# Optimization experiments

Measured on AMD Instinct MI355X. Metric: run time of the kernel, lower is better.

Reference implementation:

```python
import jax, jax.numpy as jnp
import numpy as np

B, L, D_MODEL = 8, 1024, 512
D_STATE, D_CONV, EXPAND = 16, 4, 2
D_INNER = EXPAND * D_MODEL          # 1024
DT_RANK = (D_MODEL + 15) // 16      # 32
D_FF = 4 * D_MODEL                  # 2048
EPS = 1e-12


def setup_inputs() -> dict:
    key = jax.random.key(0)
    ks = jax.random.split(key, 16)
    s = 0.02
    n = lambda k, shp: jax.random.normal(k, shp, dtype=jnp.float32) * s
    A = jnp.tile(jnp.arange(1, D_STATE + 1, dtype=jnp.float32)[None, :], (D_INNER, 1))
    return {
        "x": jax.random.normal(ks[0], (B, L, D_MODEL), dtype=jnp.float32),
        "in_proj_w": n(ks[1], (2 * D_INNER, D_MODEL)),
        "conv_w": n(ks[2], (D_INNER, 1, D_CONV)),
        "conv_b": jnp.zeros((D_INNER,), jnp.float32),
        "x_proj_w": n(ks[3], (DT_RANK + 2 * D_STATE, D_INNER)),
        "dt_proj_w": n(ks[4], (D_INNER, DT_RANK)),
        "dt_proj_b": jnp.full((D_INNER,), -4.0, jnp.float32),  # softplus(~-4) -> small dt
        "A_log": jnp.log(A),
        "D": jnp.ones((D_INNER,), jnp.float32),
        "out_proj_w": n(ks[5], (D_MODEL, D_INNER)),
        "ln1_g": jnp.ones((D_MODEL,), jnp.float32),
        "ln1_b": jnp.zeros((D_MODEL,), jnp.float32),
        "fc1_w": n(ks[6], (D_FF, D_MODEL)),
        "fc1_b": jnp.zeros((D_FF,), jnp.float32),
        "fc2_w": n(ks[7], (D_MODEL, D_FF)),
        "fc2_b": jnp.zeros((D_MODEL,), jnp.float32),
        "ln2_g": jnp.ones((D_MODEL,), jnp.float32),
        "ln2_b": jnp.zeros((D_MODEL,), jnp.float32),
    }


def _layernorm(x, g, b):
    m = jnp.mean(x, axis=-1, keepdims=True)
    v = jnp.var(x, axis=-1, keepdims=True)
    return (x - m) * jax.lax.rsqrt(v + EPS) * g + b


def _mamba(x, in_proj_w, conv_w, conv_b, x_proj_w, dt_proj_w, dt_proj_b, A_log, D, out_proj_w):
    # in_proj: [B,L,d_model] -> [B,L,2*d_inner]
    xz = jnp.einsum("bld,ed->ble", x, in_proj_w)
    u, z = jnp.split(xz, 2, axis=-1)                      # each [B,L,d_inner]
    # depthwise causal conv over time
    uc = jax.lax.conv_general_dilated(
        jnp.transpose(u, (0, 2, 1)), conv_w,
        window_strides=(1,), padding=[(D_CONV - 1, 0)],
        feature_group_count=D_INNER,
        dimension_numbers=("NCH", "OIH", "NCH"))
    u = jnp.transpose(uc, (0, 2, 1)) + conv_b             # [B,L,d_inner]
    u = jax.nn.silu(u)
    # x_proj -> dt, B, C
    x_dbl = jnp.einsum("bld,ed->ble", u, x_proj_w)
    dt, Bm, Cm = jnp.split(x_dbl, [DT_RANK, DT_RANK + D_STATE], axis=-1)
    dt = jax.nn.softplus(jnp.einsum("blr,dr->bld", dt, dt_proj_w) + dt_proj_b)  # [B,L,d_inner]
    A = -jnp.exp(A_log)                                   # [d_inner, d_state]
    deltaA = jnp.exp(dt[..., None] * A)                   # [B,L,d_inner,d_state]
    deltaBu = dt[..., None] * Bm[:, :, None, :] * u[..., None]

    def step(h, inp):
        dA_t, dBu_t, C_t = inp                            # [B,di,ds],[B,di,ds],[B,ds]
        h = h * dA_t + dBu_t
        y = jnp.einsum("bds,bs->bd", h, C_t)
        return h, y

    h0 = jnp.zeros((x.shape[0], D_INNER, D_STATE), x.dtype)
    _, ys = jax.lax.scan(step, h0, (jnp.transpose(deltaA, (1, 0, 2, 3)),
                                    jnp.transpose(deltaBu, (1, 0, 2, 3)),
                                    jnp.transpose(Cm, (1, 0, 2))))
    y = jnp.transpose(ys, (1, 0, 2)) + u * D              # [B,L,d_inner]
    y = y * jax.nn.silu(z)
    return jnp.einsum("ble,de->bld", y, out_proj_w)


def reference(x, in_proj_w, conv_w, conv_b, x_proj_w, dt_proj_w, dt_proj_b, A_log, D,
              out_proj_w, ln1_g, ln1_b, fc1_w, fc1_b, fc2_w, fc2_b, ln2_g, ln2_b):
    h = _mamba(x, in_proj_w, conv_w, conv_b, x_proj_w, dt_proj_w, dt_proj_b,
               A_log, D, out_proj_w)
    h = _layernorm(h + x, ln1_g, ln1_b)                   # dropout = identity (eval)
    # FeedForward with residual + LayerNorm
    f = jax.nn.gelu(jnp.einsum("bld,fd->blf", h, fc1_w) + fc1_b, approximate=False)
    f = jnp.einsum("blf,df->bld", f, fc2_w) + fc2_b
    return _layernorm(f + h, ln2_g, ln2_b)
```

## Files before the change

kernel.cpp:

```cpp
#include <hip/hip_runtime.h>
#include <hip/hip_bf16.h>
#include <math.h>

typedef __hip_bfloat16 bf16;
typedef unsigned short u16;
typedef unsigned int u32;
typedef __attribute__((ext_vector_type(8))) short short8;
typedef __attribute__((ext_vector_type(4))) float f32x4;
typedef __attribute__((ext_vector_type(4))) u32 u32x4;

#define B_  8
#define L_  1024
#define DM  512
#define DI  1024
#define DS  16
#define DR  32
#define DF  2048
#define M_  (B_ * L_)

__device__ __forceinline__ float b2f(bf16 x) { return __bfloat162float(x); }
__device__ __forceinline__ bf16  f2b(float x) { return __float2bfloat16(x); }
__device__ __forceinline__ u16   bu(bf16 x)  { return __builtin_bit_cast(u16, x); }
__device__ __forceinline__ float s2f(short x) { return b2f(__builtin_bit_cast(bf16, (u16)x)); }
__device__ __forceinline__ float uphi(u32 w) { return __builtin_bit_cast(float, w & 0xffff0000u); }
__device__ __forceinline__ float uplo(u32 w) { return __builtin_bit_cast(float, w << 16); }

__device__ __forceinline__ bool is_b16(const void* flag) {
    return ((const u16*)flag)[0] == 0x3F80;
}
__device__ __forceinline__ float ldr(const void* p, size_t i, bool b16) {
    return b16 ? b2f(((const bf16*)p)[i]) : ((const float*)p)[i];
}

__device__ __forceinline__ float fexp2(float x) {
#if __has_builtin(__builtin_amdgcn_exp2f)
    return __builtin_amdgcn_exp2f(x);
#else
    return __expf(x * 0.6931471805599453f);
#endif
}

__device__ __forceinline__ float fsoftplus(float v) {
    return (v > 20.f) ? v : __logf(1.f + __expf(v));
}

__device__ __forceinline__ float fgelu(float v) {
    const float x = v * 0.7071067811865475f;
    const float ax = fabsf(x);
    const float t = __builtin_amdgcn_rcpf(fmaf(0.3275911f, ax, 1.f));
    float p = fmaf(1.061405429f, t, -1.453152027f);
    p = fmaf(p, t, 1.421413741f);
    p = fmaf(p, t, -0.284496736f);
    p = fmaf(p, t, 0.254829592f);
    const float e = __expf(-ax * ax);
    float erf = 1.f - p * t * e;
    erf = (x < 0.f) ? -erf : erf;
    return 0.5f * v * (1.f + erf);
}

__device__ __forceinline__ void gload16(const bf16* g, bf16* l) {
    __builtin_amdgcn_global_load_lds(
        (const __attribute__((address_space(1))) unsigned int*)g,
        (__attribute__((address_space(3))) unsigned int*)l, 16, 0, 0);
}

__device__ __forceinline__ float fsilu(float x) {
    return x * __builtin_amdgcn_rcpf(1.f + __expf(-x));
}

#define CN0 (M_ * DM)
#define CN1 (CN0 + 2 * DI * DM)
#define CN2 (CN1 + 64 * DI)
#define CN3 (CN2 + DI * DR)
#define CN4 (CN3 + DM * DI)
#define CN5 (CN4 + DF * DM)
#define CN6 (CN5 + DM * DF)
#define CN7 (CN6 + DI * 4)
#define CN8 (CN7 + DI)
#define CN9 (CN8 + DI)
__global__ __launch_bounds__(256) void cvt_all_kernel(
    const void* s0, const void* s1, const void* s2, const void* s3,
    const void* s4, const void* s5, const void* s6, const void* s7,
    const void* s8, const void* s9,
    bf16* __restrict__ dst, const void* __restrict__ flag)
{
    const bool b16 = is_b16(flag);
    const long i = ((long)blockIdx.x * 256 + threadIdx.x) * 8;
    if (i >= CN9) return;
    const void* src; long off;
    if      (i < CN0) { src = s0; off = i; }
    else if (i < CN1) { src = s1; off = i - CN0; }
    else if (i < CN2) { src = s2; off = i - CN1; }
    else if (i < CN3) { src = s3; off = i - CN2; }
    else if (i < CN4) { src = s4; off = i - CN3; }
    else if (i < CN5) { src = s5; off = i - CN4; }
    else if (i < CN6) { src = s6; off = i - CN5; }
    else if (i < CN7) { src = s7; off = i - CN6; }
    else if (i < CN8) { src = s8; off = i - CN7; }
    else              { src = s9; off = i - CN8; }
    if (b16) {
        *(short8*)(dst + i) = *(const short8*)((const bf16*)src + off);
    } else {
        const float* f = (const float*)src + off;
        const f32x4 a = *(const f32x4*)f;
        const f32x4 b = *(const f32x4*)(f + 4);
        short8 o;
#pragma unroll
        for (int k = 0; k < 4; ++k) {
            o[k]     = (short)bu(f2b(a[k]));
            o[k + 4] = (short)bu(f2b(b[k]));
        }
        *(short8*)(dst + i) = o;
    }
}

template <int BM, int BN, int NT, int ACT, int PACK>
__global__ __launch_bounds__(NT) void mfma_gemm(
    const bf16* __restrict__ A, int lda,
    const bf16* __restrict__ W, int ldw,
    const void* __restrict__ bias,
    bf16* __restrict__ C, int ldc,
    int K, const void* __restrict__ flag,
    void* __restrict__ pk, void* __restrict__ pk2,
    const bf16* __restrict__ uin)
{
    constexpr int WN = (BN >= 128) ? 2 : 1;
    constexpr int CA = BM * 4 / NT;
    constexpr int CB = BN * 4 / NT;
    constexpr int BUF = (BM + BN) * 32;
    __shared__ __align__(16) bf16 smem[2 * BUF];
    const int tid  = threadIdx.x;
    const int wave = tid >> 6, lane = tid & 63;
    const int quad = lane >> 4, l16 = lane & 15;
    const u32 gx  = gridDim.x;
    const u32 nwg = gx * gridDim.y;
    const u32 lid = blockIdx.y * gx + blockIdx.x;
    const u32 swz = (lid & 7) * (nwg >> 3) + (lid >> 3);
    const int bm = (int)(swz / gx) * BM, bn = (int)(swz % gx) * BN;
    const int wm = (wave / WN) * 64, wn = (wave % WN) * 64;

    f32x4 acc[4][4];
#pragma unroll
    for (int i = 0; i < 4; ++i)
#pragma unroll
        for (int j = 0; j < 4; ++j) acc[i][j] = (f32x4){0.f, 0.f, 0.f, 0.f};

    auto load_tile = [&](int k0, int p) {
        bf16* As = smem + p * BUF;
        bf16* Ws = As + BM * 32;
#pragma unroll
        for (int j = 0; j < CA; ++j) {
            const int e = j * NT + tid;
            gload16(A + (size_t)(bm + (e >> 2)) * lda + k0 + (e & 3) * 8, As + e * 8);
        }
#pragma unroll
        for (int j = 0; j < CB; ++j) {
            const int e = j * NT + tid;
            gload16(W + (size_t)(bn + (e >> 2)) * ldw + k0 + (e & 3) * 8, Ws + e * 8);
        }
    };

    const int NIT = K >> 5;
    load_tile(0, 0);
    for (int it = 0; it < NIT; ++it) {
        __syncthreads();
        if (it + 1 < NIT) load_tile((it + 1) << 5, (it + 1) & 1);
        const bf16* As = smem + (it & 1) * BUF;
        const bf16* Ws = As + BM * 32;
        short8 af[4], wf[4];
#pragma unroll
        for (int mt = 0; mt < 4; ++mt)
            af[mt] = *(const short8*)(As + (wm + mt * 16 + l16) * 32 + quad * 8);
#pragma unroll
        for (int nt = 0; nt < 4; ++nt)
            wf[nt] = *(const short8*)(Ws + (wn + nt * 16 + l16) * 32 + quad * 8);
#pragma unroll
        for (int mt = 0; mt < 4; ++mt)
#pragma unroll
            for (int nt = 0; nt < 4; ++nt)
                acc[mt][nt] = __builtin_amdgcn_mfma_f32_16x16x32_bf16(
                    af[mt], wf[nt], acc[mt][nt], 0, 0, 0);
    }

    const bool b16 = bias ? is_b16(flag) : false;
#pragma unroll
    for (int nt = 0; nt < 4; ++nt) {
        const int col = bn + wn + nt * 16 + l16;
        const float bv = bias ? ldr(bias, col, b16) : 0.f;
#pragma unroll
        for (int mt = 0; mt < 4; ++mt)
#pragma unroll
            for (int i = 0; i < 4; ++i) {
                const int row = bm + wm + mt * 16 + quad * 4 + i;
                float v = acc[mt][nt][i] + bv;
                if (ACT == 1) v = fsoftplus(v);
                else if (ACT == 2) v = fgelu(v);
                C[(size_t)row * ldc + col] = f2b(v);
            }
    }
    if (PACK == 2) {
#pragma unroll
        for (int mt = 0; mt < 4; ++mt)
#pragma unroll
            for (int i = 0; i < 4; ++i) {
                const int row = bm + wm + mt * 16 + quad * 4 + i;
                ((float*)pk)[(size_t)row * 16 + l16]  = acc[mt][2][i];
                ((float*)pk2)[(size_t)row * 16 + l16] = acc[mt][3][i];
            }
    }
}

__global__ __launch_bounds__(256) void conv_silu_kernel(
    const bf16* __restrict__ xz,
    const bf16* __restrict__ cw,
    const bf16* __restrict__ cb,
    const bf16* __restrict__ Dw,
    bf16* __restrict__ u,
    u32* __restrict__ ug)
{
    const int t  = blockIdx.x * 256 + threadIdx.x;
    const long t8 = (long)t * 8;
    const int d8  = (int)(t8 & (DI - 1));
    const int row = (int)(t8 >> 10);
    const int l   = row & (L_ - 1);

    short8 wraw[4];
#pragma unroll
    for (int k = 0; k < 4; ++k)
        wraw[k] = *(const short8*)(cw + (size_t)d8 * 4 + k * 8);
    const short8 cbv = *(const short8*)(cb + d8);
    const short8 dv  = *(const short8*)(Dw + d8);

    float acc[8];
#pragma unroll
    for (int i = 0; i < 8; ++i) acc[i] = s2f(cbv[i]);
#pragma unroll
    for (int j = 0; j < 4; ++j) {
        const int ls = l - 3 + j;
        if (ls >= 0) {
            const short8 xv = *(const short8*)(xz + (size_t)(row - 3 + j) * (2 * DI) + d8);
#pragma unroll
            for (int i = 0; i < 8; ++i) {
                const int f = i * 4 + j;
                acc[i] += s2f(wraw[f >> 3][f & 7]) * s2f(xv[i]);
            }
        }
    }
    const short8 zv = *(const short8*)(xz + (size_t)row * (2 * DI) + DI + d8);
    short8 us;
    u32x4 g0, g1;
#pragma unroll
    for (int i = 0; i < 8; ++i) {
        const float uv = fsilu(acc[i]);
        us[i] = (short)bu(f2b(uv));
        const float gz = fsilu(s2f(zv[i]));
        const float g2 = uv * s2f(dv[i]) * gz;
        const u32 p = ((u32)bu(f2b(g2)) << 16) | bu(f2b(gz));
        if (i < 4) g0[i] = p; else g1[i - 4] = p;
    }
    *(short8*)(u + t8) = us;
    *(u32x4*)(ug + t8) = g0;
    *(u32x4*)(ug + t8 + 4) = g1;
}

__global__ __launch_bounds__(256) void scan_kernel(
    const bf16* __restrict__ xdbl,
    const bf16* __restrict__ u,
    const float* __restrict__ Bf,
    const float* __restrict__ Cf,
    const u32* __restrict__ ug,
    const void* __restrict__ A_log,
    const bf16* __restrict__ dtw,
    const void* __restrict__ dt_b,
    bf16* __restrict__ y,
    const void* __restrict__ flag)
{
    const bool b16 = is_b16(flag);
    const int tid = threadIdx.x;
    const int lane = tid & 63;
    const int s  = lane & 15;
    const int dl = tid >> 4;
    const int quad = dl & 3;
    const int v = tid >> 6;
    const int b = blockIdx.x >> 6, dch = blockIdx.x & 63;
    const int d0 = dch * 16, d = d0 + dl;
    const float AcL = -__expf(ldr(A_log, (size_t)d * DS + s, b16))
                      * 1.4426950408889634f;

    const short8 wfrag = *(const short8*)(dtw + (size_t)(d0 + s) * DR + quad * 8);
    const float dtb = ldr(dt_b, d0 + s, b16);

    __shared__ __align__(16) float dt_s[16][68];
    __shared__ __align__(16) float du_s[16][68];
    __shared__ __align__(16) float B_s[16][68];
    __shared__ __align__(16) float C_s[16][68];
    __shared__ u32 ug_s[16][68];
    __shared__ bf16 y_s[16][72];
    __shared__ float p_s[16][16][33];

    const int c16 = tid & 15, r16 = tid >> 4;
    float rB[4], rC[4];
    u32 rug[4];
    short8 rxd;
    u16 ru4[4];
    const size_t base = (size_t)b * L_;

    auto load_chunk = [&](int l0) {
#pragma unroll
        for (int j = 0; j < 4; ++j) {
            const size_t row = base + l0 + r16 + 16 * j;
            rug[j] = ug[row * DI + d0 + c16];
            rB[j]  = Bf[row * 16 + c16];
            rC[j]  = Cf[row * 16 + c16];
        }
        rxd = *(const short8*)(xdbl + (size_t)(base + l0 + v * 16 + s) * 64
                               + quad * 8);
#pragma unroll
        for (int i = 0; i < 4; ++i)
            ru4[i] = ((const u16*)u)[(size_t)(base + l0 + v * 16 + quad * 4 + i)
                                     * DI + d0 + s];
    };
    auto store_chunk = [&]() {
#pragma unroll
        for (int j = 0; j < 4; ++j) {
            ug_s[c16][r16 + 16 * j] = rug[j];
            B_s[c16][r16 + 16 * j]  = rB[j];
            C_s[c16][r16 + 16 * j]  = rC[j];
        }
        f32x4 a0 = __builtin_amdgcn_mfma_f32_16x16x32_bf16(
            rxd, wfrag, (f32x4){0.f, 0.f, 0.f, 0.f}, 0, 0, 0);
        f32x4 dtv, duv;
#pragma unroll
        for (int i = 0; i < 4; ++i) {
            const float t = fsoftplus(a0[i] + dtb);
            dtv[i] = t;
            duv[i] = t * s2f((short)ru4[i]);
        }
        *(f32x4*)&dt_s[s][v * 16 + quad * 4] = dtv;
        *(f32x4*)&du_s[s][v * 16 + quad * 4] = duv;
    };

    float h = 0.f;
    float* const prow = &p_s[dl][s][0];
    load_chunk(0);
    for (int c = 0; c < 16; ++c) {
        store_chunk();
        __syncthreads();
        if (c < 15) load_chunk((c + 1) * 64);
#pragma unroll
        for (int g = 0; g < 2; ++g) {
#pragma unroll
            for (int w2 = 0; w2 < 2; ++w2) {
                const int w = g * 2 + w2;
                f32x4 dtw4[4], duw[4], bw[4], cw[4];
#pragma unroll
                for (int q = 0; q < 4; ++q) {
                    dtw4[q] = *(const f32x4*)&dt_s[dl][w * 16 + q * 4];
                    duw[q]  = *(const f32x4*)&du_s[dl][w * 16 + q * 4];
                    bw[q]   = *(const f32x4*)&B_s[s][w * 16 + q * 4];
                    cw[q]   = *(const f32x4*)&C_s[s][w * 16 + q * 4];
                }
#pragma unroll
                for (int t = 0; t < 16; ++t) {
                    const float e = fexp2(dtw4[t >> 2][t & 3] * AcL);
                    h = fmaf(h, e, duw[t >> 2][t & 3] * bw[t >> 2][t & 3]);
                    prow[w2 * 16 + t] = h * cw[t >> 2][t & 3];
                }
            }
            asm volatile("s_waitcnt lgkmcnt(0)" ::: "memory");
#pragma unroll
            for (int w2 = 0; w2 < 2; ++w2) {
                const int w = g * 2 + w2;
                const u32 ugw = ug_s[dl][w * 16 + s];
                float pr[16];
#pragma unroll
                for (int k = 0; k < 16; ++k) pr[k] = p_s[dl][k][w2 * 16 + s];
#pragma unroll
                for (int o = 8; o >= 1; o >>= 1)
#pragma unroll
                    for (int i = 0; i < o; ++i) pr[i] += pr[i + o];
                y_s[dl][w * 16 + s] = f2b(fmaf(pr[0], uplo(ugw), uphi(ugw)));
            }
        }
        __syncthreads();
#pragma unroll
        for (int j = 0; j < 4; ++j) {
            const size_t row = base + c * 64 + r16 + 16 * j;
            y[row * DI + d0 + c16] = y_s[c16][r16 + 16 * j];
        }
    }
}

template <int RMODE, int OMODE>
__global__ __launch_bounds__(256) void ln_kernel(
    const bf16* __restrict__ inp,
    const bf16* __restrict__ res,
    const void* __restrict__ g,
    const void* __restrict__ bb,
    void* __restrict__ out,
    const void* __restrict__ flag)
{
    const bool b16 = is_b16(flag);
    const int wv = threadIdx.x >> 6, lane = threadIdx.x & 63;
    const int row = blockIdx.x * 4 + wv;
    const size_t off = (size_t)row * DM;
    const int e = lane * 8;

    float v[8];
    const short8 iv = *(const short8*)(inp + off + e);
    const short8 rv = *(const short8*)(res + off + e);
#pragma unroll
    for (int i = 0; i < 8; ++i) v[i] = s2f(iv[i]) + s2f(rv[i]);

    float sum = 0.f, sq = 0.f;
#pragma unroll
    for (int i = 0; i < 8; ++i) { sum += v[i]; sq += v[i] * v[i]; }
#pragma unroll
    for (int o = 32; o >= 1; o >>= 1) {
        sum += __shfl_xor(sum, o);
        sq  += __shfl_xor(sq, o);
    }
    const float m = sum * (1.f / DM);
    const float var = sq * (1.f / DM) - m * m;
    const float inv = rsqrtf(fmaxf(var, 0.f) + 1e-12f);

    float gv[8], bv[8];
    if (b16) {
        const short8 gg = *(const short8*)((const bf16*)g + e);
        const short8 bg = *(const short8*)((const bf16*)bb + e);
#pragma unroll
        for (int i = 0; i < 8; ++i) { gv[i] = s2f(gg[i]); bv[i] = s2f(bg[i]); }
    } else {
        const float* gf = (const float*)g + e;
        const float* bf = (const float*)bb + e;
        const f32x4 g0 = *(const f32x4*)gf, g1 = *(const f32x4*)(gf + 4);
        const f32x4 b0 = *(const f32x4*)bf, b1 = *(const f32x4*)(bf + 4);
#pragma unroll
        for (int i = 0; i < 8; ++i) {
            gv[i] = i < 4 ? g0[i] : g1[i - 4];
            bv[i] = i < 4 ? b0[i] : b1[i - 4];
        }
    }
    float o[8];
#pragma unroll
    for (int i = 0; i < 8; ++i) o[i] = (v[i] - m) * inv * gv[i] + bv[i];

    if (OMODE == 2 && !b16) {
        f32x4 o0, o1;
#pragma unroll
        for (int i = 0; i < 4; ++i) { o0[i] = o[i]; o1[i] = o[i + 4]; }
        *(f32x4*)((float*)out + off + e) = o0;
        *(f32x4*)((float*)out + off + e + 4) = o1;
    } else {
        short8 os;
#pragma unroll
        for (int i = 0; i < 8; ++i) os[i] = (short)bu(f2b(o[i]));
        *(short8*)((bf16*)out + off + e) = os;
    }
}

extern "C" void kernel_launch(void* const* d_in, const int* in_sizes, int n_in,
                              void* d_out, int out_size, void* d_ws, size_t ws_size,
                              hipStream_t stream)
{
    (void)in_sizes; (void)n_in; (void)out_size; (void)ws_size;
    const void* x       = d_in[0];
    const void* in_w    = d_in[1];
    const void* conv_w  = d_in[2];
    const void* conv_b  = d_in[3];
    const void* xproj_w = d_in[4];
    const void* dt_w    = d_in[5];
    const void* dt_b    = d_in[6];
    const void* A_log   = d_in[7];
    const void* Dw      = d_in[8];
    const void* out_w   = d_in[9];
    const void* ln1_g   = d_in[10];
    const void* ln1_b   = d_in[11];
    const void* fc1_w   = d_in[12];
    const void* fc1_b   = d_in[13];
    const void* fc2_w   = d_in[14];
    const void* fc2_b   = d_in[15];
    const void* ln2_g   = d_in[16];
    const void* ln2_b   = d_in[17];
    const void* flag    = ln1_g;

    bf16* xb    = (bf16*)d_ws;
    bf16* inwb  = xb    + (size_t)M_ * DM;
    bf16* xpwb  = inwb  + (size_t)2 * DI * DM;
    bf16* dtwb  = xpwb  + (size_t)64 * DI;
    bf16* outwb = dtwb  + (size_t)DI * DR;
    bf16* fc1wb = outwb + (size_t)DM * DI;
    bf16* fc2wb = fc1wb + (size_t)DF * DM;
    bf16* cwb   = fc2wb + (size_t)DM * DF;
    bf16* cbb   = cwb   + (size_t)DI * 4;
    bf16* dwb   = cbb   + (size_t)DI;
    bf16* xz    = dwb   + (size_t)DI;
    bf16* u     = xz    + (size_t)M_ * 2 * DI;
    bf16* xdbl  = u     + (size_t)M_ * DI;
    float* dtf  = (float*)(xdbl + (size_t)M_ * 64);
    u32*  ugp   = (u32*)(dtf + (size_t)M_ * DI);
    float* Bfp  = (float*)(ugp + (size_t)M_ * DI);
    bf16* yb    = (bf16*)(Bfp + (size_t)M_ * 16);
    bf16* hb    = yb    + (size_t)M_ * DI;
    float* Cfp  = (float*)hb;
    bf16* mo    = (bf16*)dtf;
    bf16* fb    = xz;
    bf16* f2b_  = yb;

    dim3 blk(256);
    cvt_all_kernel<<<dim3((CN9 / 8 + 255) / 256), blk, 0, stream>>>(
        x, in_w, xproj_w, dt_w, out_w, fc1_w, fc2_w, conv_w, conv_b, Dw,
        xb, flag);

    mfma_gemm<128, 128, 256, 0, 0><<<dim3(16, 64), blk, 0, stream>>>(
        xb, DM, inwb, DM, nullptr, xz, 2 * DI, DM, flag, nullptr, nullptr, nullptr);
    conv_silu_kernel<<<dim3(M_ * DI / 8 / 256), blk, 0, stream>>>(
        xz, cwb, cbb, dwb, u, ugp);
    mfma_gemm<128, 64, 128, 0, 2><<<dim3(1, 64), dim3(128), 0, stream>>>(
        u, DI, xpwb, DI, nullptr, xdbl, 64, DI, flag, Bfp, Cfp, nullptr);
    scan_kernel<<<dim3(B_ * 64), blk, 0, stream>>>(
        xdbl, u, Bfp, Cfp, ugp, A_log, dtwb, dt_b, yb, flag);
    mfma_gemm<128, 128, 256, 0, 0><<<dim3(4, 64), blk, 0, stream>>>(
        yb, DI, outwb, DI, nullptr, mo, DM, DI, flag, nullptr, nullptr, nullptr);
    ln_kernel<1, 1><<<dim3(M_ / 4), blk, 0, stream>>>(
        mo, xb, ln1_g, ln1_b, hb, flag);
    mfma_gemm<128, 128, 256, 2, 0><<<dim3(16, 64), blk, 0, stream>>>(
        hb, DM, fc1wb, DM, fc1_b, fb, DF, DM, flag, nullptr, nullptr, nullptr);
    mfma_gemm<128, 128, 256, 0, 0><<<dim3(4, 64), blk, 0, stream>>>(
        fb, DF, fc2wb, DF, fc2_b, f2b_, DM, DF, flag, nullptr, nullptr, nullptr);
    ln_kernel<1, 2><<<dim3(M_ / 4), blk, 0, stream>>>(
        f2b_, hb, ln2_g, ln2_b, d_out, flag);
}
```

Baseline: 326.8 us.

## Add 256x256-tile 8-wave pipelined GEMM for in_proj and fc1

Introduces a new GEMM kernel using 256x256 output tiles with 512 threads, a 128KB LDS double buffer split into half-tiles, staged prefetch interleaved with MFMA quarters, setprio, and an XCD-aware workgroup swizzle. It replaces the 128x128 GEMM for the in_proj and fc1 (with bias+GELU) projections. The aim is higher data reuse per LDS load and better overlap of global loads with matrix math. The tradeoff is one block per CU because of the large LDS footprint, a high accumulator register count, and only 256 workgroups, which may underfill the GPU.

Measured after the change: 348.4 us. +6.6%, slower.

```diff
diff --git a/kernel.cpp b/kernel.cpp
--- a/kernel.cpp
+++ b/kernel.cpp
@@ -114,6 +114,127 @@
     }
 }
 
+template <int ACT, int BIAS>
+__global__ __launch_bounds__(512) void gemm8p(
+    const bf16* __restrict__ A, int lda,
+    const bf16* __restrict__ W, int ldw,
+    const void* __restrict__ bias,
+    bf16* __restrict__ C, int ldc,
+    int K, const void* __restrict__ flag)
+{
+    __shared__ __align__(16) bf16 smem[65536];
+    const int tid  = threadIdx.x;
+    const int wave = tid >> 6, lane = tid & 63;
+    const int quad = lane >> 4, l16 = lane & 15;
+    const int wr = (wave >> 2) * 64;
+    const int wc = (wave & 3) * 32;
+    const u32 gx  = gridDim.x;
+    const u32 nwg = gx * gridDim.y;
+    const u32 lid = blockIdx.y * gx + blockIdx.x;
+    const u32 swz = (lid & 7) * (nwg >> 3) + (lid >> 3);
+    const int bm = (int)(swz / gx) * 256, bn = (int)(swz % gx) * 256;
+
+    auto slot = [&](int p, int ab, int hf) -> bf16* {
+        return smem + (size_t)((((p << 1) | ab) << 1) | hf) * 8192;
+    };
+    auto stage_half = [&](int kt, int ab, int hf) {
+        bf16* dst = slot(kt & 1, ab, hf);
+        const bf16* src = ab ? W : A;
+        const int ld    = ab ? ldw : lda;
+        const int rbase = (ab ? bn : bm) + hf * 128;
+        const int k0 = kt * 64;
+#pragma unroll
+        for (int j = 0; j < 2; ++j) {
+            const int e = j * 512 + tid;
+            gload16(src + (size_t)(rbase + (e >> 3)) * ld + k0 + (e & 7) * 8,
+                    dst + e * 8);
+        }
+    };
+
+    f32x4 acc[4][4][2];
+#pragma unroll
+    for (int q = 0; q < 4; ++q)
+#pragma unroll
+        for (int mf = 0; mf < 4; ++mf)
+#pragma unroll
+            for (int nf = 0; nf < 2; ++nf)
+                acc[q][mf][nf] = (f32x4){0.f, 0.f, 0.f, 0.f};
+
+    const int NIT = K >> 6;
+    stage_half(0, 0, 0); stage_half(0, 1, 0);
+    stage_half(0, 0, 1); stage_half(0, 1, 1);
+    stage_half(1, 0, 0); stage_half(1, 1, 0);
+    asm volatile("s_waitcnt vmcnt(4)" ::: "memory");
+    __builtin_amdgcn_s_barrier();
+    __builtin_amdgcn_sched_barrier(0);
+
+    for (int kt = 0; kt < NIT; ++kt) {
+        const int p = kt & 1;
+#pragma unroll
+        for (int q = 0; q < 4; ++q) {
+            const bf16* Ah = slot(p, 0, q >> 1);
+            const bf16* Bh = slot(p, 1, q & 1);
+            short8 af[4][2], bfr[2][2];
+#pragma unroll
+            for (int mf = 0; mf < 4; ++mf)
+#pragma unroll
+                for (int ks = 0; ks < 2; ++ks)
+                    af[mf][ks] = *(const short8*)(
+                        Ah + (wr + mf * 16 + l16) * 64 + ks * 32 + quad * 8);
+#pragma unroll
+            for (int nf = 0; nf < 2; ++nf)
+#pragma unroll
+                for (int ks = 0; ks < 2; ++ks)
+                    bfr[nf][ks] = *(const short8*)(
+                        Bh + (wc + nf * 16 + l16) * 64 + ks * 32 + quad * 8);
+            if      (q == 0) { if (kt + 1 < NIT) stage_half(kt + 1, 0, 1); }
+            else if (q == 1) { if (kt + 1 < NIT) stage_half(kt + 1, 1, 1); }
+            else if (q == 2) { if (kt + 2 < NIT) stage_half(kt + 2, 0, 0); }
+            else             { if (kt + 2 < NIT) stage_half(kt + 2, 1, 0); }
+            __builtin_amdgcn_sched_barrier(0);
+            __builtin_amdgcn_s_barrier();
+            __builtin_amdgcn_sched_barrier(0);
+            __builtin_amdgcn_s_setprio(1);
+#pragma unroll
+            for (int mf = 0; mf < 4; ++mf)
+#pragma unroll
+                for (int nf = 0; nf < 2; ++nf)
+#pragma unroll
+                    for (int ks = 0; ks < 2; ++ks)
+                        acc[q][mf][nf] = __builtin_amdgcn_mfma_f32_16x16x32_bf16(
+                            af[mf][ks], bfr[nf][ks], acc[q][mf][nf], 0, 0, 0);
+            __builtin_amdgcn_s_setprio(0);
+            __builtin_amdgcn_sched_barrier(0);
+            if (q == 3 && kt + 1 < NIT) {
+                if (kt + 2 < NIT)
+                    asm volatile("s_waitcnt vmcnt(4)" ::: "memory");
+                else
+                    asm volatile("s_waitcnt vmcnt(0)" ::: "memory");
+            }
+            __builtin_amdgcn_s_barrier();
+            __builtin_amdgcn_sched_barrier(0);
+        }
+    }
+
+    const bool b16f = BIAS ? is_b16(flag) : false;
+#pragma unroll
+    for (int q = 0; q < 4; ++q)
+#pragma unroll
+        for (int nf = 0; nf < 2; ++nf) {
+            const int col = bn + (q & 1) * 128 + wc + nf * 16 + l16;
+            const float bv = BIAS ? ldr(bias, col, b16f) : 0.f;
+#pragma unroll
+            for (int mf = 0; mf < 4; ++mf)
+#pragma unroll
+                for (int i = 0; i < 4; ++i) {
+                    const int row = bm + (q >> 1) * 128 + wr + mf * 16 + quad * 4 + i;
+                    float v = acc[q][mf][nf][i] + bv;
+                    if (ACT == 2) v = fgelu(v);
+                    C[(size_t)row * ldc + col] = f2b(v);
+                }
+        }
+}
+
 template <int BM, int BN, int NT, int ACT, int PACK>
 __global__ __launch_bounds__(NT) void mfma_gemm(
     const bf16* __restrict__ A, int lda,
@@ -512,8 +633,8 @@
         x, in_w, xproj_w, dt_w, out_w, fc1_w, fc2_w, conv_w, conv_b, Dw,
         xb, flag);
 
-    mfma_gemm<128, 128, 256, 0, 0><<<dim3(16, 64), blk, 0, stream>>>(
-        xb, DM, inwb, DM, nullptr, xz, 2 * DI, DM, flag, nullptr, nullptr, nullptr);
+    gemm8p<0, 0><<<dim3(8, 32), dim3(512), 0, stream>>>(
+        xb, DM, inwb, DM, nullptr, xz, 2 * DI, DM, flag);
     conv_silu_kernel<<<dim3(M_ * DI / 8 / 256), blk, 0, stream>>>(
         xz, cwb, cbb, dwb, u, ugp);
     mfma_gemm<128, 64, 128, 0, 2><<<dim3(1, 64), dim3(128), 0, stream>>>(
@@ -524,8 +645,8 @@
         yb, DI, outwb, DI, nullptr, mo, DM, DI, flag, nullptr, nullptr, nullptr);
     ln_kernel<1, 1><<<dim3(M_ / 4), blk, 0, stream>>>(
         mo, xb, ln1_g, ln1_b, hb, flag);
-    mfma_gemm<128, 128, 256, 2, 0><<<dim3(16, 64), blk, 0, stream>>>(
-        hb, DM, fc1wb, DM, fc1_b, fb, DF, DM, flag, nullptr, nullptr, nullptr);
+    gemm8p<2, 1><<<dim3(8, 32), dim3(512), 0, stream>>>(
+        hb, DM, fc1wb, DM, fc1_b, fb, DF, DM, flag);
     mfma_gemm<128, 128, 256, 0, 0><<<dim3(4, 64), blk, 0, stream>>>(
         fb, DF, fc2wb, DF, fc2_b, f2b_, DM, DF, flag, nullptr, nullptr, nullptr);
     ln_kernel<1, 2><<<dim3(M_ / 4), blk, 0, stream>>>(
```
